# Kernel tuning notes

Measured on AMD Instinct MI355X. Metric: run time of the kernel, lower is better.

## Reference

```python
import jax, jax.numpy as jnp
import numpy as np

N = 100000      # nodes
E = 1600000     # edges
IN = 4          # input_size
H = 128         # hidden_channels
R = 20          # num_robots
OUT = 2         # output_size


def setup_inputs() -> dict:
    key = jax.random.key(0)
    ks = jax.random.split(key, 9)
    x = jax.random.normal(ks[0], (N, IN), dtype=jnp.float32)
    edge_index = jax.random.randint(ks[1], (2, E), 0, N, dtype=jnp.int32)
    batch = jnp.zeros((N,), dtype=jnp.int32)  # single graph
    # GCNConv weights (glorot-ish) and biases
    W1 = jax.random.normal(ks[2], (IN, H), dtype=jnp.float32) / np.sqrt(IN)
    b1 = jnp.zeros((H,), dtype=jnp.float32)
    W2 = jax.random.normal(ks[3], (H, H), dtype=jnp.float32) / np.sqrt(H)
    b2 = jnp.zeros((H,), dtype=jnp.float32)
    Wfc = jax.random.normal(ks[4], (H, OUT * R), dtype=jnp.float32) / np.sqrt(H)
    bfc = jnp.zeros((OUT * R,), dtype=jnp.float32)
    return {"x": x, "edge_index": edge_index, "batch": batch,
            "W1": W1, "b1": b1, "W2": W2, "b2": b2, "Wfc": Wfc, "bfc": bfc}


def gcn_conv(x, W, b, src, dst, n):
    # PyG GCNConv: h = x @ W, symmetric deg^-1/2 norm (self-loops already in src/dst),
    # aggregate messages at dst, then add bias.
    h = x @ W                                                     # [n, H_out]
    deg = jax.ops.segment_sum(jnp.ones(src.shape[0], h.dtype), dst, num_segments=n)
    dinv = jnp.where(deg > 0, jax.lax.rsqrt(deg), 0.0)            # [n]
    norm = dinv[src] * dinv[dst]                                  # [E+n]
    out = jax.ops.segment_sum(h[src] * norm[:, None], dst, num_segments=n)
    return out + b


def reference(x, edge_index, batch, W1, b1, W2, b2, Wfc, bfc):
    n = x.shape[0]
    loops = jnp.arange(n, dtype=edge_index.dtype)
    src = jnp.concatenate([edge_index[0], loops])   # add self-loops (GCNConv default)
    dst = jnp.concatenate([edge_index[1], loops])

    h = jnp.tanh(gcn_conv(x, W1, b1, src, dst, n))
    h = jnp.tanh(gcn_conv(h, W2, b2, src, dst, n))

    # global_mean_pool over batch (single graph)
    num_graphs = 1
    sums = jax.ops.segment_sum(h, batch, num_segments=num_graphs)           # [G, H]
    cnt = jax.ops.segment_sum(jnp.ones((n,), h.dtype), batch, num_segments=num_graphs)
    pooled = sums / jnp.maximum(cnt, 1.0)[:, None]

    vel = (pooled @ Wfc + bfc).reshape(-1, R, OUT)                          # [G, R, 2]

    # in_size = number of nodes with both first two features nonzero
    in_size = jnp.sum((x[:, 0] != 0.0) & (x[:, 1] != 0.0))
    mask = (jnp.arange(R) < in_size)[None, :, None]
    return jnp.where(mask, vel, 0.0)
```

## Files before the change

kernel.cpp:

```cpp
#include <hip/hip_runtime.h>
#include <hip/hip_fp16.h>

#define NN 100000
#define NE 1600000
#define INF 4
#define H 128
#define RR 20
#define OUTF 2
#define NB 782
#define NBP 784
#define EPB 16384
#define NBLK ((NE + EPB - 1) / EPB)
#define ASPLIT 4

typedef unsigned int uint32;
typedef __attribute__((ext_vector_type(8))) short short8;
typedef __attribute__((ext_vector_type(4))) float f32x4;

__device__ inline uint32 pack_f16(float x, float y) {
    return (uint32)__half_as_ushort(__float2half(x)) |
           ((uint32)__half_as_ushort(__float2half(y)) << 16);
}
__device__ inline __half2 bc_h2(uint32 u) {
    union { uint32 u; __half2 h; } c; c.u = u; return c.h;
}

__global__ void __launch_bounds__(256) k_hist(const int* __restrict__ dst,
                                              int* __restrict__ histG) {
    __shared__ int h[NB];
    int b = blockIdx.x, t = threadIdx.x;
    for (int i = t; i < NB; i += 256) h[i] = 0;
    __syncthreads();
    int e0 = b * EPB, eend = min(e0 + EPB, NE);
    for (int e = e0 + t; e < eend; e += 256) atomicAdd(&h[dst[e] >> 7], 1);
    __syncthreads();
    for (int i = t; i < NB; i += 256) histG[b * NBP + i] = h[i];
}

__global__ void __launch_bounds__(1024) k_scan(const int* __restrict__ histG,
                                               int* __restrict__ offs,
                                               int* __restrict__ bbase) {
    __shared__ int sm[1024];
    int t = threadIdx.x;
    int run = 0;
    if (t < NB) {
        for (int j = 0; j < NBLK; ++j) {
            int v = histG[j * NBP + t];
            offs[j * NBP + t] = run;
            run += v;
        }
    }
    sm[t] = (t < NB) ? run : 0;
    __syncthreads();
    for (int off = 1; off < 1024; off <<= 1) {
        int u = (t >= off) ? sm[t - off] : 0;
        __syncthreads();
        sm[t] += u;
        __syncthreads();
    }
    if (t < NB) bbase[t] = sm[t] - run;
    if (t == 0) bbase[NB] = NE;
}

__global__ void __launch_bounds__(256) k_scat2(const int* __restrict__ src,
                                               const int* __restrict__ dst,
                                               const int* __restrict__ offs,
                                               const int* __restrict__ bbase,
                                               uint32* __restrict__ data) {
    __shared__ int cur[NB];
    int b = blockIdx.x, t = threadIdx.x;
    for (int i = t; i < NB; i += 256) cur[i] = offs[b * NBP + i] + bbase[i];
    __syncthreads();
    int e0 = b * EPB, eend = min(e0 + EPB, NE);
    for (int e = e0 + t; e < eend; e += 256) {
        int s = src[e], d = dst[e];
        int p = atomicAdd(&cur[d >> 7], 1);
        data[p] = ((uint32)s << 7) | (uint32)(d & 127);
    }
}

__global__ void __launch_bounds__(256) k_build(const uint32* __restrict__ data,
                                               const int* __restrict__ bbase,
                                               const float* __restrict__ x,
                                               int* __restrict__ csr_off,
                                               int* __restrict__ csr_cnt,
                                               int* __restrict__ csr_src,
                                               float* __restrict__ dinv,
                                               float4* __restrict__ xd,
                                               int* __restrict__ in_size) {
    __shared__ int hist[128], pfx[128], curs[128];
    int bkt = blockIdx.x;
    int t = threadIdx.x;
    int rbeg = bbase[bkt], rend = bbase[bkt + 1];
    if (t < 128) hist[t] = 0;
    __syncthreads();
    for (int j = rbeg + t; j < rend; j += 256)
        atomicAdd(&hist[data[j] & 127], 1);
    __syncthreads();
    if (t < 128) pfx[t] = hist[t];
    __syncthreads();
    for (int off = 1; off < 128; off <<= 1) {
        int u = (t < 128 && t >= off) ? pfx[t - off] : 0;
        __syncthreads();
        if (t < 128) pfx[t] += u;
        __syncthreads();
    }
    int nodeCount = min(128, NN - bkt * 128);
    bool pred = false;
    if (t < nodeCount) {
        int gi = bkt * 128 + t;
        int excl = rbeg + pfx[t] - hist[t];
        csr_off[gi] = excl;
        csr_cnt[gi] = hist[t];
        curs[t] = excl;
        float di = rsqrtf((float)(hist[t] + 1));
        dinv[gi] = di;
        const float4 xv = *(const float4*)(x + (size_t)gi * INF);
        xd[gi] = make_float4(xv.x * di, xv.y * di, xv.z * di, xv.w * di);
        pred = (xv.x != 0.f) && (xv.y != 0.f);
    }
    unsigned long long m = __ballot(pred);
    if ((t & 63) == 0) {
        int c = __popcll(m);
        if (c) atomicAdd(in_size, c);
    }
    __syncthreads();
    for (int j = rbeg + t; j < rend; j += 256) {
        uint32 r = data[j];
        int p = atomicAdd(&curs[r & 127], 1);
        csr_src[p] = (int)(r >> 7);
    }
}

__global__ void __launch_bounds__(256) k_aggx4(const uint32* __restrict__ data,
                                               const int* __restrict__ bbase,
                                               const float4* __restrict__ xd,
                                               float* __restrict__ Axpart) {
    __shared__ float acc[128][4];
    int bkt = blockIdx.x >> 2, sp = blockIdx.x & 3;
    int t = threadIdx.x;
    if (t < 128) { acc[t][0] = 0.f; acc[t][1] = 0.f; acc[t][2] = 0.f; acc[t][3] = 0.f; }
    int rbeg = bbase[bkt], rend = bbase[bkt + 1];
    int len = rend - rbeg;
    int q0 = rbeg + ((long long)len * sp >> 2);
    int q1 = rbeg + ((long long)len * (sp + 1) >> 2);
    __syncthreads();
    for (int j = q0 + t; j < q1; j += 256) {
        uint32 r = data[j];
        int s = (int)(r >> 7), dl = (int)(r & 127);
        const float4 v = xd[s];
        atomicAdd(&acc[dl][0], v.x);
        atomicAdd(&acc[dl][1], v.y);
        atomicAdd(&acc[dl][2], v.z);
        atomicAdd(&acc[dl][3], v.w);
    }
    __syncthreads();
    float* dstp = Axpart + (size_t)blockIdx.x * 512;
    for (int i = t; i < 512; i += 256) dstp[i] = ((const float*)acc)[i];
}

__global__ void __launch_bounds__(256) k_mm1c(const float* __restrict__ Axpart,
                                              const float4* __restrict__ xd,
                                              const float* __restrict__ dinv,
                                              const float* __restrict__ W1,
                                              const float* __restrict__ b1,
                                              uint32* __restrict__ Yp) {
    __shared__ float axs[128][4];
    __shared__ float ds[128];
    __shared__ float w1s[4][128];
    __shared__ float b1s[128];
    int bkt = blockIdx.x;
    int t = threadIdx.x;
    if (t < 128) b1s[t] = b1[t];
    ((float*)w1s)[t] = W1[t];
    ((float*)w1s)[256 + t] = W1[256 + t];
    int nodeCount = min(128, NN - bkt * 128);
    if (t < nodeCount) {
        int gi = bkt * 128 + t;
        float4 a = xd[gi];
        #pragma unroll
        for (int sp = 0; sp < 4; ++sp) {
            const float4 p = *(const float4*)(Axpart + ((size_t)(bkt * 4 + sp)) * 512 + t * 4);
            a.x += p.x; a.y += p.y; a.z += p.z; a.w += p.w;
        }
        float di = dinv[gi];
        axs[t][0] = a.x * di; axs[t][1] = a.y * di;
        axs[t][2] = a.z * di; axs[t][3] = a.w * di;
        ds[t] = di;
    }
    __syncthreads();
    int nbase = bkt * 128;
    #pragma unroll
    for (int rep = 0; rep < 32; ++rep) {
        int flat = rep * 256 + t;
        int node = flat >> 6;
        int fp = flat & 63;
        int gi = nbase + node;
        if (gi < NN) {
            float a0 = axs[node][0], a1 = axs[node][1];
            float a2 = axs[node][2], a3 = axs[node][3];
            float di = ds[node];
            int f0 = fp * 2;
            float d0 = b1s[f0]     + a0 * w1s[0][f0]     + a1 * w1s[1][f0]
                                   + a2 * w1s[2][f0]     + a3 * w1s[3][f0];
            float d1 = b1s[f0 + 1] + a0 * w1s[0][f0 + 1] + a1 * w1s[1][f0 + 1]
                                   + a2 * w1s[2][f0 + 1] + a3 * w1s[3][f0 + 1];
            Yp[(size_t)gi * 64 + fp] = pack_f16(tanhf(d0) * di, tanhf(d1) * di);
        }
    }
}

__global__ void k_aggy(const uint32* __restrict__ Yp, const int* __restrict__ csr_off,
                       const int* __restrict__ csr_cnt, const int* __restrict__ csr_src,
                       const float* __restrict__ dinv, uint32* __restrict__ Zp) {
    int wid = threadIdx.x >> 6;
    int lane = threadIdx.x & 63;
    int i = blockIdx.x * 4 + wid;
    if (i >= NN) return;
    int b = csr_off[i];
    int n = csr_cnt[i];
    int eg = lane >> 4, seg = lane & 15;

    __half2 h0 = bc_h2(0u), h1 = bc_h2(0u), h2 = bc_h2(0u), h3 = bc_h2(0u);
    int j = 0;
    for (; j + 16 <= n; j += 16) {
        int s0 = csr_src[b + j + eg];
        int s1 = csr_src[b + j + 4 + eg];
        int s2 = csr_src[b + j + 8 + eg];
        int s3 = csr_src[b + j + 12 + eg];
        uint4 v0 = *(const uint4*)(Yp + (size_t)s0 * 64 + seg * 4);
        uint4 v1 = *(const uint4*)(Yp + (size_t)s1 * 64 + seg * 4);
        uint4 v2 = *(const uint4*)(Yp + (size_t)s2 * 64 + seg * 4);
        uint4 v3 = *(const uint4*)(Yp + (size_t)s3 * 64 + seg * 4);
        h0 = __hadd2(h0, bc_h2(v0.x)); h1 = __hadd2(h1, bc_h2(v0.y));
        h2 = __hadd2(h2, bc_h2(v0.z)); h3 = __hadd2(h3, bc_h2(v0.w));
        h0 = __hadd2(h0, bc_h2(v1.x)); h1 = __hadd2(h1, bc_h2(v1.y));
        h2 = __hadd2(h2, bc_h2(v1.z)); h3 = __hadd2(h3, bc_h2(v1.w));
        h0 = __hadd2(h0, bc_h2(v2.x)); h1 = __hadd2(h1, bc_h2(v2.y));
        h2 = __hadd2(h2, bc_h2(v2.z)); h3 = __hadd2(h3, bc_h2(v2.w));
        h0 = __hadd2(h0, bc_h2(v3.x)); h1 = __hadd2(h1, bc_h2(v3.y));
        h2 = __hadd2(h2, bc_h2(v3.z)); h3 = __hadd2(h3, bc_h2(v3.w));
    }
    for (; j + 8 <= n; j += 8) {
        int s0 = csr_src[b + j + eg];
        int s1 = csr_src[b + j + 4 + eg];
        uint4 v0 = *(const uint4*)(Yp + (size_t)s0 * 64 + seg * 4);
        uint4 v1 = *(const uint4*)(Yp + (size_t)s1 * 64 + seg * 4);
        h0 = __hadd2(h0, bc_h2(v0.x)); h1 = __hadd2(h1, bc_h2(v0.y));
        h2 = __hadd2(h2, bc_h2(v0.z)); h3 = __hadd2(h3, bc_h2(v0.w));
        h0 = __hadd2(h0, bc_h2(v1.x)); h1 = __hadd2(h1, bc_h2(v1.y));
        h2 = __hadd2(h2, bc_h2(v1.z)); h3 = __hadd2(h3, bc_h2(v1.w));
    }
    for (; j < n; j += 4) {
        int jj = j + eg;
        bool valid = jj < n;
        int s = valid ? csr_src[b + jj] : i;
        uint4 v = *(const uint4*)(Yp + (size_t)s * 64 + seg * 4);
        if (valid) {
            h0 = __hadd2(h0, bc_h2(v.x)); h1 = __hadd2(h1, bc_h2(v.y));
            h2 = __hadd2(h2, bc_h2(v.z)); h3 = __hadd2(h3, bc_h2(v.w));
        }
    }
    {
        uint4 v = *(const uint4*)(Yp + (size_t)i * 64 + seg * 4);
        if (eg == 0) {
            h0 = __hadd2(h0, bc_h2(v.x)); h1 = __hadd2(h1, bc_h2(v.y));
            h2 = __hadd2(h2, bc_h2(v.z)); h3 = __hadd2(h3, bc_h2(v.w));
        }
    }
    float a[8];
    { float2 f = __half22float2(h0); a[0] = f.x; a[1] = f.y; }
    { float2 f = __half22float2(h1); a[2] = f.x; a[3] = f.y; }
    { float2 f = __half22float2(h2); a[4] = f.x; a[5] = f.y; }
    { float2 f = __half22float2(h3); a[6] = f.x; a[7] = f.y; }
    #pragma unroll
    for (int m = 0; m < 8; ++m) {
        a[m] += __shfl_xor(a[m], 16, 64);
        a[m] += __shfl_xor(a[m], 32, 64);
    }
    if (eg == 0) {
        float di = dinv[i];
        uint4 o;
        o.x = pack_f16(a[0] * di, a[1] * di);
        o.y = pack_f16(a[2] * di, a[3] * di);
        o.z = pack_f16(a[4] * di, a[5] * di);
        o.w = pack_f16(a[6] * di, a[7] * di);
        *(uint4*)(Zp + (size_t)i * 64 + seg * 4) = o;
    }
}

__global__ void __launch_bounds__(256) k_mm2pool(
    const uint32* __restrict__ Zp, const float* __restrict__ W2,
    const float* __restrict__ b2, float* __restrict__ pooled) {
    int tid = threadIdx.x;
    int wid = tid >> 6, lane = tid & 63;
    int nsub = lane & 15;
    int kg = lane >> 4;
    int fbase = wid * 32;

    short8 Bh[2][4], Bl[2][4];
    #pragma unroll
    for (int c = 0; c < 2; ++c) {
        #pragma unroll
        for (int ks = 0; ks < 4; ++ks) {
            short8 h, l;
            #pragma unroll
            for (int i = 0; i < 8; ++i) {
                float w = W2[(size_t)(ks * 32 + kg * 8 + i) * H + (fbase + c * 16 + nsub)];
                __half hh = __float2half(w);
                float wl = w - __half2float(hh);
                __half hl = __float2half(wl);
                h[i] = (short)__half_as_ushort(hh);
                l[i] = (short)__half_as_ushort(hl);
            }
            Bh[c][ks] = h;
            Bl[c][ks] = l;
        }
    }
    float bb0 = b2[fbase + nsub];
    float bb1 = b2[fbase + 16 + nsub];
    float pool0 = 0.f, pool1 = 0.f;

    const int ntiles = NN / 16;
    const int stride = (int)gridDim.x;
    int t = (int)blockIdx.x;

    short8 A[4];
    if (t < ntiles) {
        const uint32* rp = Zp + (size_t)(t * 16 + nsub) * 64 + kg * 4;
        #pragma unroll
        for (int ks = 0; ks < 4; ++ks) A[ks] = *(const short8*)(rp + ks * 16);
    }
    while (t < ntiles) {
        int tn = t + stride;
        short8 An[4];
        if (tn < ntiles) {
            const uint32* rp = Zp + (size_t)(tn * 16 + nsub) * 64 + kg * 4;
            #pragma unroll
            for (int ks = 0; ks < 4; ++ks) An[ks] = *(const short8*)(rp + ks * 16);
        }
        {
            f32x4 acch0 = {0.f,0.f,0.f,0.f}, accl0 = {0.f,0.f,0.f,0.f};
            f32x4 acch1 = {0.f,0.f,0.f,0.f}, accl1 = {0.f,0.f,0.f,0.f};
            #pragma unroll
            for (int ks = 0; ks < 4; ++ks) {
                acch0 = __builtin_amdgcn_mfma_f32_16x16x32_f16(A[ks], Bh[0][ks], acch0, 0, 0, 0);
                accl0 = __builtin_amdgcn_mfma_f32_16x16x32_f16(A[ks], Bl[0][ks], accl0, 0, 0, 0);
                acch1 = __builtin_amdgcn_mfma_f32_16x16x32_f16(A[ks], Bh[1][ks], acch1, 0, 0, 0);
                accl1 = __builtin_amdgcn_mfma_f32_16x16x32_f16(A[ks], Bl[1][ks], accl1, 0, 0, 0);
            }
            #pragma unroll
            for (int r = 0; r < 4; ++r) {
                pool0 += tanhf(acch0[r] + accl0[r] + bb0);
                pool1 += tanhf(acch1[r] + accl1[r] + bb1);
            }
        }
        #pragma unroll
        for (int ks = 0; ks < 4; ++ks) A[ks] = An[ks];
        t = tn;
    }

    pool0 += __shfl_xor(pool0, 16, 64);
    pool0 += __shfl_xor(pool0, 32, 64);
    pool1 += __shfl_xor(pool1, 16, 64);
    pool1 += __shfl_xor(pool1, 32, 64);
    if (kg == 0) {
        atomicAdd(&pooled[fbase + nsub], pool0);
        atomicAdd(&pooled[fbase + 16 + nsub], pool1);
    }
}

__global__ void k_final(const float* __restrict__ pooled, const float* __restrict__ Wfc,
                        const float* __restrict__ bfc, const int* __restrict__ in_size,
                        float* __restrict__ out) {
    int t = threadIdx.x;
    if (t >= RR * OUTF) return;
    const float invn = 1.0f / (float)NN;
    float a = bfc[t];
    for (int k = 0; k < H; ++k) a += (pooled[k] * invn) * Wfc[k * (RR * OUTF) + t];
    int r = t >> 1;
    out[t] = (r < *in_size) ? a : 0.f;
}

extern "C" void kernel_launch(void* const* d_in, const int* in_sizes, int n_in,
                              void* d_out, int out_size, void* d_ws, size_t ws_size,
                              hipStream_t stream) {
    const float* x   = (const float*)d_in[0];
    const int*   ei  = (const int*)d_in[1];
    const float* W1  = (const float*)d_in[3];
    const float* b1  = (const float*)d_in[4];
    const float* W2  = (const float*)d_in[5];
    const float* b2  = (const float*)d_in[6];
    const float* Wfc = (const float*)d_in[7];
    const float* bfc = (const float*)d_in[8];
    float* out = (float*)d_out;

    const int* srcp = ei;
    const int* dstp = ei + NE;

    char* ws = (char*)d_ws;
    size_t off = 0;
    auto alloc = [&](size_t bytes) { void* p = ws + off; off += (bytes + 511) & ~(size_t)511; return p; };
    float*  pooled  = (float*)alloc(H * 4);
    int*    in_size = (int*)alloc(64);
    int*    histG   = (int*)alloc((size_t)NBLK * NBP * 4);
    int*    offs    = (int*)alloc((size_t)NBLK * NBP * 4);
    int*    bbase   = (int*)alloc(((size_t)NB + 1) * 4);
    uint32* data    = (uint32*)alloc((size_t)NE * 4);
    float*  dinv    = (float*)alloc((size_t)NN * 4);
    float4* xd      = (float4*)alloc((size_t)NN * 16);
    int*    csr_off = (int*)alloc((size_t)NN * 4);
    int*    csr_cnt = (int*)alloc((size_t)NN * 4);
    int*    csr_src = (int*)alloc((size_t)NE * 4);
    float*  Axpart  = (float*)alloc((size_t)NB * ASPLIT * 512 * 4);
    uint32* Yp      = (uint32*)alloc((size_t)NN * 64 * 4);
    uint32* Zp      = (uint32*)alloc((size_t)NN * 64 * 4);
    (void)off; (void)ws_size; (void)in_sizes; (void)n_in; (void)out_size;

    const int nbW = (NN + 3) / 4;

    hipMemsetAsync(pooled, 0, 1024, stream);
    k_hist<<<NBLK, 256, 0, stream>>>(dstp, histG);
    k_scan<<<1, 1024, 0, stream>>>(histG, offs, bbase);
    k_scat2<<<NBLK, 256, 0, stream>>>(srcp, dstp, offs, bbase, data);
    k_build<<<NB, 256, 0, stream>>>(data, bbase, x, csr_off, csr_cnt, csr_src, dinv, xd, in_size);
    k_aggx4<<<NB * ASPLIT, 256, 0, stream>>>(data, bbase, xd, Axpart);
    k_mm1c<<<NB, 256, 0, stream>>>(Axpart, xd, dinv, W1, b1, Yp);
    k_aggy<<<nbW, 256, 0, stream>>>(Yp, csr_off, csr_cnt, csr_src, dinv, Zp);
    k_mm2pool<<<512, 256, 0, stream>>>(Zp, W2, b2, pooled);
    k_final<<<1, 64, 0, stream>>>(pooled, Wfc, bfc, in_size, out);
}
```

Before: 309.9 us.

## Fuse layer-1 aggregation and W1 transform into one CSR-based kernel

Replaces the bucketed shared-memory atomic aggregation and the separate W1 matmul kernel with one kernel. In it, 16-lane groups gather each node's neighbours through the CSR, reduce with shuffles, apply W1, bias and tanh, and write packed fp16 rows with vector stores. This removes a kernel launch, the Axpart partial-sum buffer round trip and LDS atomic contention. In exchange it relies on the CSR being built and does per-node gathers with variable degree, which may leave some lanes idle.

```diff
diff --git a/kernel.cpp b/kernel.cpp
--- a/kernel.cpp
+++ b/kernel.cpp
@@ -11,7 +11,6 @@
 #define NBP 784
 #define EPB 16384
 #define NBLK ((NE + EPB - 1) / EPB)
-#define ASPLIT 4
 
 typedef unsigned int uint32;
 typedef __attribute__((ext_vector_type(8))) short short8;
@@ -132,82 +131,56 @@
     }
 }
 
-__global__ void __launch_bounds__(256) k_aggx4(const uint32* __restrict__ data,
-                                               const int* __restrict__ bbase,
-                                               const float4* __restrict__ xd,
-                                               float* __restrict__ Axpart) {
-    __shared__ float acc[128][4];
-    int bkt = blockIdx.x >> 2, sp = blockIdx.x & 3;
-    int t = threadIdx.x;
-    if (t < 128) { acc[t][0] = 0.f; acc[t][1] = 0.f; acc[t][2] = 0.f; acc[t][3] = 0.f; }
-    int rbeg = bbase[bkt], rend = bbase[bkt + 1];
-    int len = rend - rbeg;
-    int q0 = rbeg + ((long long)len * sp >> 2);
-    int q1 = rbeg + ((long long)len * (sp + 1) >> 2);
-    __syncthreads();
-    for (int j = q0 + t; j < q1; j += 256) {
-        uint32 r = data[j];
-        int s = (int)(r >> 7), dl = (int)(r & 127);
-        const float4 v = xd[s];
-        atomicAdd(&acc[dl][0], v.x);
-        atomicAdd(&acc[dl][1], v.y);
-        atomicAdd(&acc[dl][2], v.z);
-        atomicAdd(&acc[dl][3], v.w);
-    }
-    __syncthreads();
-    float* dstp = Axpart + (size_t)blockIdx.x * 512;
-    for (int i = t; i < 512; i += 256) dstp[i] = ((const float*)acc)[i];
-}
-
-__global__ void __launch_bounds__(256) k_mm1c(const float* __restrict__ Axpart,
-                                              const float4* __restrict__ xd,
-                                              const float* __restrict__ dinv,
-                                              const float* __restrict__ W1,
-                                              const float* __restrict__ b1,
-                                              uint32* __restrict__ Yp) {
-    __shared__ float axs[128][4];
-    __shared__ float ds[128];
+__global__ void __launch_bounds__(256) k_l1(const int* __restrict__ csr_off,
+                                            const int* __restrict__ csr_cnt,
+                                            const int* __restrict__ csr_src,
+                                            const float4* __restrict__ xd,
+                                            const float* __restrict__ dinv,
+                                            const float* __restrict__ W1,
+                                            const float* __restrict__ b1,
+                                            uint32* __restrict__ Yp) {
     __shared__ float w1s[4][128];
     __shared__ float b1s[128];
-    int bkt = blockIdx.x;
     int t = threadIdx.x;
     if (t < 128) b1s[t] = b1[t];
     ((float*)w1s)[t] = W1[t];
     ((float*)w1s)[256 + t] = W1[256 + t];
-    int nodeCount = min(128, NN - bkt * 128);
-    if (t < nodeCount) {
-        int gi = bkt * 128 + t;
-        float4 a = xd[gi];
-        #pragma unroll
-        for (int sp = 0; sp < 4; ++sp) {
-            const float4 p = *(const float4*)(Axpart + ((size_t)(bkt * 4 + sp)) * 512 + t * 4);
-            a.x += p.x; a.y += p.y; a.z += p.z; a.w += p.w;
-        }
-        float di = dinv[gi];
-        axs[t][0] = a.x * di; axs[t][1] = a.y * di;
-        axs[t][2] = a.z * di; axs[t][3] = a.w * di;
-        ds[t] = di;
-    }
-    __syncthreads();
-    int nbase = bkt * 128;
+    __syncthreads();
+    int wid = t >> 6, lane = t & 63;
+    int l16 = lane & 15, grp = lane >> 4;
+    int i = blockIdx.x * 16 + wid * 4 + grp;
+    int b = csr_off[i], n = csr_cnt[i];
+    float a0 = 0.f, a1 = 0.f, a2 = 0.f, a3 = 0.f;
+    for (int j = l16; j < n; j += 16) {
+        int s = csr_src[b + j];
+        const float4 v = xd[s];
+        a0 += v.x; a1 += v.y; a2 += v.z; a3 += v.w;
+    }
     #pragma unroll
-    for (int rep = 0; rep < 32; ++rep) {
-        int flat = rep * 256 + t;
-        int node = flat >> 6;
-        int fp = flat & 63;
-        int gi = nbase + node;
-        if (gi < NN) {
-            float a0 = axs[node][0], a1 = axs[node][1];
-            float a2 = axs[node][2], a3 = axs[node][3];
-            float di = ds[node];
-            int f0 = fp * 2;
-            float d0 = b1s[f0]     + a0 * w1s[0][f0]     + a1 * w1s[1][f0]
-                                   + a2 * w1s[2][f0]     + a3 * w1s[3][f0];
-            float d1 = b1s[f0 + 1] + a0 * w1s[0][f0 + 1] + a1 * w1s[1][f0 + 1]
-                                   + a2 * w1s[2][f0 + 1] + a3 * w1s[3][f0 + 1];
-            Yp[(size_t)gi * 64 + fp] = pack_f16(tanhf(d0) * di, tanhf(d1) * di);
-        }
-    }
+    for (int off = 1; off < 16; off <<= 1) {
+        a0 += __shfl_xor(a0, off, 64);
+        a1 += __shfl_xor(a1, off, 64);
+        a2 += __shfl_xor(a2, off, 64);
+        a3 += __shfl_xor(a3, off, 64);
+    }
+    const float4 self = xd[i];
+    float di = dinv[i];
+    a0 = (a0 + self.x) * di;
+    a1 = (a1 + self.y) * di;
+    a2 = (a2 + self.z) * di;
+    a3 = (a3 + self.w) * di;
+    int f0 = l16 * 8;
+    uint4 o;
+    #pragma unroll
+    for (int q = 0; q < 4; ++q) {
+        int f = f0 + q * 2;
+        float d0 = b1s[f]     + a0 * w1s[0][f]     + a1 * w1s[1][f]
+                              + a2 * w1s[2][f]     + a3 * w1s[3][f];
+        float d1 = b1s[f + 1] + a0 * w1s[0][f + 1] + a1 * w1s[1][f + 1]
+                              + a2 * w1s[2][f + 1] + a3 * w1s[3][f + 1];
+        (&o.x)[q] = pack_f16(tanhf(d0) * di, tanhf(d1) * di);
+    }
+    *(uint4*)(Yp + (size_t)i * 64 + l16 * 4) = o;
 }
 
 __global__ void k_aggy(const uint32* __restrict__ Yp, const int* __restrict__ csr_off,
@@ -412,7 +385,6 @@
     int*    csr_off = (int*)alloc((size_t)NN * 4);
     int*    csr_cnt = (int*)alloc((size_t)NN * 4);
     int*    csr_src = (int*)alloc((size_t)NE * 4);
-    float*  Axpart  = (float*)alloc((size_t)NB * ASPLIT * 512 * 4);
     uint32* Yp      = (uint32*)alloc((size_t)NN * 64 * 4);
     uint32* Zp      = (uint32*)alloc((size_t)NN * 64 * 4);
     (void)off; (void)ws_size; (void)in_sizes; (void)n_in; (void)out_size;
@@ -424,8 +396,7 @@
     k_scan<<<1, 1024, 0, stream>>>(histG, offs, bbase);
     k_scat2<<<NBLK, 256, 0, stream>>>(srcp, dstp, offs, bbase, data);
     k_build<<<NB, 256, 0, stream>>>(data, bbase, x, csr_off, csr_cnt, csr_src, dinv, xd, in_size);
-    k_aggx4<<<NB * ASPLIT, 256, 0, stream>>>(data, bbase, xd, Axpart);
-    k_mm1c<<<NB, 256, 0, stream>>>(Axpart, xd, dinv, W1, b1, Yp);
+    k_l1<<<NN / 16, 256, 0, stream>>>(csr_off, csr_cnt, csr_src, xd, dinv, W1, b1, Yp);
     k_aggy<<<nbW, 256, 0, stream>>>(Yp, csr_off, csr_cnt, csr_src, dinv, Zp);
     k_mm2pool<<<512, 256, 0, stream>>>(Zp, W2, b2, pooled);
     k_final<<<1, 64, 0, stream>>>(pooled, Wfc, bfc, in_size, out);
```

Result: faster. 277.6 us (-10.4%).
